# Optimization experiments

Hardware: AMD Instinct MI355X
Metric: run time of the kernel (lower is better)

Reference implementation:

```python
import jax, jax.numpy as jnp
import numpy as np

B, S, D = 2, 2048, 1024
H, HD = 16, 64  # H*HD == D (required by proj layer)
SCALE = D ** -0.5  # NOTE: original scales by full input dim (x.shape[-1]), not head dim


def setup_inputs() -> dict:
    key = jax.random.key(0)
    ks = jax.random.split(key, 7)
    std = D ** -0.5
    x = jax.random.normal(ks[0], (B, S, D), dtype=jnp.float32)
    # per-head projection weights, stacked: [H, D, HD] so x @ Wq[h] == Linear(D->HD)
    Wq = jax.random.normal(ks[1], (H, D, HD), dtype=jnp.float32) * std
    Wk = jax.random.normal(ks[2], (H, D, HD), dtype=jnp.float32) * std
    Wv = jax.random.normal(ks[3], (H, D, HD), dtype=jnp.float32) * std
    # output projection Linear(D, D) with bias
    Wp = jax.random.normal(ks[4], (D, D), dtype=jnp.float32) * std
    bp = jax.random.normal(ks[5], (D,), dtype=jnp.float32) * 0.01
    return {"x": x, "Wq": Wq, "Wk": Wk, "Wv": Wv, "Wp": Wp, "bp": bp}


def reference(x, Wq, Wk, Wv, Wp, bp):
    # All heads see the full x (atsp=False path). Dropout in eval mode (identity).
    q = jnp.einsum('bsd,hde->bhse', x, Wq)  # [B,H,S,HD]
    k = jnp.einsum('bsd,hde->bhse', x, Wk)
    v = jnp.einsum('bsd,hde->bhse', x, Wv)
    scores = jnp.einsum('bhse,bhte->bhst', q, k) * SCALE  # [B,H,S,S]
    causal = jnp.tril(jnp.ones((S, S), dtype=bool))
    scores = jnp.where(causal, scores, -jnp.inf)
    attn = jax.nn.softmax(scores, axis=-1)
    out = jnp.einsum('bhst,bhte->bhse', attn, v)          # [B,H,S,HD]
    # concat heads along last dim in head order: [B,S,H*HD]
    out = out.transpose(0, 2, 1, 3).reshape(B, S, H * HD)
    return out @ Wp.T + bp
```

## Files before the change

### kernel.cpp

```cpp
#include <hip/hip_runtime.h>

typedef __bf16 bf16x8 __attribute__((ext_vector_type(8)));
typedef __bf16 bf16x4 __attribute__((ext_vector_type(4)));
typedef float f32x4 __attribute__((ext_vector_type(4)));
typedef unsigned short u16;
typedef unsigned int u32;

static constexpr int kS = 2048, kD = 1024, kHD = 64;
static constexpr float kQScale = 0.03125f * 1.44269504f;

__device__ __forceinline__ u16 f2bf(float f) {
  union { float f; u32 u; } v; v.f = f;
  u32 r = v.u + 0x7FFFu + ((v.u >> 16) & 1u);
  return (u16)(r >> 16);
}
__device__ __forceinline__ float bf2f(u16 u) {
  union { u32 u; float f; } v; v.u = ((u32)u) << 16;
  return v.f;
}
__device__ __forceinline__ u32 pk2(float a, float b) {
  return (u32)f2bf(a) | ((u32)f2bf(b) << 16);
}
__device__ __forceinline__ f32x4 mfma16(bf16x8 a, bf16x8 b, f32x4 c) {
  return __builtin_amdgcn_mfma_f32_16x16x32_bf16(a, b, c, 0, 0, 0);
}
__device__ __forceinline__ void gld16(u16* lds, const u16* g) {
  __builtin_amdgcn_global_load_lds(
      (const __attribute__((address_space(1))) u32*)g,
      (__attribute__((address_space(3))) u32*)lds, 16, 0, 0);
}

union Pack8 { u16 u[8]; uint4 v; };

__global__ void detect_dtype_kernel(const u16* __restrict__ xr, int* __restrict__ flag) {
  __shared__ int cnt;
  if (threadIdx.x == 0) cnt = 0;
  __syncthreads();
  int c = 0;
  for (int i = threadIdx.x; i < 2048; i += 256) {
    int ex = (xr[i] >> 7) & 0xFF;
    if (ex >= 134) c++;
  }
  if (c) atomicAdd(&cnt, c);
  __syncthreads();
  if (threadIdx.x == 0) flag[0] = (cnt > 16) ? 1 : 0;
}

__global__ void cast_all_kernel(const void* Wq, const void* Wk, const void* Wv,
                                const void* Wp, const void* x,
                                u16* __restrict__ Wt, u16* __restrict__ Wpb,
                                u16* __restrict__ xb, const int* __restrict__ flag) {
  bool f32m = flag[0] != 0;
  int bid = blockIdx.x;
  int t = threadIdx.x;
  __shared__ float Ts[64][65];
  if (bid < 768) {
    int u = bid >> 4;
    int d0 = (bid & 15) * 64;
    int w = u >> 4, h = u & 15;
    const void* srcv = (w == 0) ? Wq : (w == 1) ? Wk : Wv;
    const float* sf = (const float*)srcv + (size_t)h * kD * kHD;
    const u16*   sb = (const u16*)srcv + (size_t)h * kD * kHD;
    int row = t >> 4;
    int c4 = (t & 15) * 4;
    for (int rr = 0; rr < 64; rr += 16) {
      int r = rr + row;
      if (f32m) {
        float4 v = *(const float4*)&sf[(size_t)(d0 + r) * kHD + c4];
        Ts[r][c4 + 0] = v.x; Ts[r][c4 + 1] = v.y; Ts[r][c4 + 2] = v.z; Ts[r][c4 + 3] = v.w;
      } else {
        const u16* p = &sb[(size_t)(d0 + r) * kHD + c4];
        Ts[r][c4 + 0] = bf2f(p[0]); Ts[r][c4 + 1] = bf2f(p[1]);
        Ts[r][c4 + 2] = bf2f(p[2]); Ts[r][c4 + 3] = bf2f(p[3]);
      }
    }
    __syncthreads();
    for (int rr = 0; rr < 64; rr += 16) {
      int e = rr + row;
      uint2 pk;
      pk.x = pk2(Ts[c4 + 0][e], Ts[c4 + 1][e]);
      pk.y = pk2(Ts[c4 + 2][e], Ts[c4 + 3][e]);
      *(uint2*)&Wt[(size_t)u * (kHD * kD) + (size_t)e * kD + d0 + c4] = pk;
    }
  } else if (bid < 1792) {
    int i = ((bid - 768) * 256 + t) * 4;
    if (f32m) {
      float4 v = *(const float4*)((const float*)Wp + i);
      uint2 pk; pk.x = pk2(v.x, v.y); pk.y = pk2(v.z, v.w);
      *(uint2*)&Wpb[i] = pk;
    } else {
      *(uint2*)&Wpb[i] = *(const uint2*)((const u16*)Wp + i);
    }
  } else {
    size_t i = ((size_t)(bid - 1792) * 256 + t) * 8;
    if (f32m) {
      const float* xf = (const float*)x;
      float4 a = *(const float4*)&xf[i];
      float4 b = *(const float4*)&xf[i + 4];
      Pack8 pk;
      pk.u[0] = f2bf(a.x); pk.u[1] = f2bf(a.y); pk.u[2] = f2bf(a.z); pk.u[3] = f2bf(a.w);
      pk.u[4] = f2bf(b.x); pk.u[5] = f2bf(b.y); pk.u[6] = f2bf(b.z); pk.u[7] = f2bf(b.w);
      *(uint4*)&xb[i] = pk.v;
    } else {
      *(uint4*)&xb[i] = *(const uint4*)((const u16*)x + i);
    }
  }
}

__global__ __launch_bounds__(256) void qkv_gemm_kernel(const u16* __restrict__ xb,
    const u16* __restrict__ Wt, u16* __restrict__ Q, u16* __restrict__ K,
    u16* __restrict__ Vt) {
  int m0 = blockIdx.x * 128;
  int n0 = blockIdx.y * 128;
  int w = (int)(blockIdx.y >> 3);
  const u16 *Ap, *Bp; int a0, b0;
  if (w == 2) { Ap = xb; a0 = m0; Bp = Wt; b0 = n0; }
  else        { Ap = Wt; a0 = n0; Bp = xb; b0 = m0; }
  int t = threadIdx.x;
  int wv = t >> 6, l = t & 63;
  int fr = l & 15, fq = l >> 4;
  int wI = (wv >> 1) * 64, wJ = (wv & 1) * 64;
  __shared__ __align__(16) u16 As[128][64];
  __shared__ __align__(16) u16 Bs[128][64];
  int srow = l >> 3, scol = (l & 7) * 8;
  f32x4 acc[4][4];
#pragma unroll
  for (int ii = 0; ii < 4; ++ii)
#pragma unroll
    for (int jj = 0; jj < 4; ++jj)
      for (int i = 0; i < 4; ++i) acc[ii][jj][i] = 0.f;

  for (int kb = 0; kb < kD / 64; ++kb) {
    int k0 = kb * 64;
    __syncthreads();
#pragma unroll
    for (int j = 0; j < 4; ++j) {
      int row = (wv * 4 + j) * 8 + srow;
      gld16(&As[row][scol], &Ap[(size_t)(a0 + row) * kD + k0 + scol]);
      gld16(&Bs[row][scol], &Bp[(size_t)(b0 + row) * kD + k0 + scol]);
    }
    __syncthreads();
    bf16x8 af[4][2], bg[4][2];
#pragma unroll
    for (int ii = 0; ii < 4; ++ii) {
      af[ii][0] = *(const bf16x8*)&As[wI + ii * 16 + fr][fq * 8];
      af[ii][1] = *(const bf16x8*)&As[wI + ii * 16 + fr][32 + fq * 8];
    }
#pragma unroll
    for (int jj = 0; jj < 4; ++jj) {
      bg[jj][0] = *(const bf16x8*)&Bs[wJ + jj * 16 + fr][fq * 8];
      bg[jj][1] = *(const bf16x8*)&Bs[wJ + jj * 16 + fr][32 + fq * 8];
    }
#pragma unroll
    for (int ii = 0; ii < 4; ++ii)
#pragma unroll
      for (int jj = 0; jj < 4; ++jj) {
        acc[ii][jj] = mfma16(af[ii][0], bg[jj][0], acc[ii][jj]);
        acc[ii][jj] = mfma16(af[ii][1], bg[jj][1], acc[ii][jj]);
      }
  }

  if (w == 2) {
    int uh = wv & 1;
    int u = 2 * blockIdx.y + uh;
    int h = u & 15;
#pragma unroll
    for (int jj = 0; jj < 4; ++jj) {
      int e = jj * 16 + fr;
#pragma unroll
      for (int ii = 0; ii < 4; ++ii) {
        int m = m0 + wI + ii * 16 + fq * 4;
        int b = m >> 11, s0 = m & 2047;
        int bh = b * 16 + h;
        *(bf16x4*)&Vt[((size_t)bh * kHD + e) * kS + s0] =
            __builtin_convertvector(acc[ii][jj], bf16x4);
      }
    }
  } else {
    int uh = wv >> 1;
    int u = 2 * blockIdx.y + uh;
    int h = u & 15;
    bool isQ = (w == 0);
    u16* dst = isQ ? Q : K;
#pragma unroll
    for (int jj = 0; jj < 4; ++jj) {
      int m = m0 + wJ + jj * 16 + fr;
      int b = m >> 11, s = m & 2047;
      int bh = b * 16 + h;
      size_t rowb = ((size_t)bh * kS + s) * kHD;
#pragma unroll
      for (int ii = 0; ii < 4; ++ii) {
        int e0 = ii * 16 + fq * 4;
        f32x4 v = acc[ii][jj];
        if (isQ) v *= kQScale;
        *(bf16x4*)&dst[rowb + e0] = __builtin_convertvector(v, bf16x4);
      }
    }
  }
}

__global__ __launch_bounds__(256) void attn_kernel(const u16* __restrict__ Q,
    const u16* __restrict__ K, const u16* __restrict__ Vt, u16* __restrict__ cat) {
  int qb = 31 - (int)(blockIdx.x >> 5);
  int bh = (int)(blockIdx.x & 31);
  int q0 = qb * 64;
  int t = threadIdx.x;
  int wv = t >> 6, l = t & 63;
  int fr = l & 15, fq = l >> 4;
  __shared__ __align__(16) u16 Ks[64][72];
  __shared__ __align__(16) u16 Vs[64][72];
  __shared__ __align__(16) u16 Ps[4][16][72];
  const u16* Qb = Q + (size_t)bh * kS * kHD;
  const u16* Kb = K + (size_t)bh * kS * kHD;
  const u16* Vb = Vt + (size_t)bh * kHD * kS;

  int qrow = q0 + wv * 16 + fr;
  bf16x8 qf0 = *(const bf16x8*)&Qb[(size_t)qrow * kHD + fq * 8];
  bf16x8 qf1 = *(const bf16x8*)&Qb[(size_t)qrow * kHD + 32 + fq * 8];

  f32x4 O[4];
#pragma unroll
  for (int nt = 0; nt < 4; ++nt) for (int i = 0; i < 4; ++i) O[nt][i] = 0.f;
  float lsum = 0.f;

  int srow0 = t >> 3, scol = (t & 7) * 8;
  int srow1 = srow0 + 32;
  uint4 kr0 = *(const uint4*)&Kb[(size_t)srow0 * kHD + scol];
  uint4 kr1 = *(const uint4*)&Kb[(size_t)srow1 * kHD + scol];
  uint4 vr0 = *(const uint4*)&Vb[(size_t)srow0 * kS + scol];
  uint4 vr1 = *(const uint4*)&Vb[(size_t)srow1 * kS + scol];

  for (int tt = 0; tt <= qb; ++tt) {
    int t0 = tt * 64;
    __syncthreads();
    *(uint4*)&Ks[srow0][scol] = kr0;
    *(uint4*)&Ks[srow1][scol] = kr1;
    *(uint4*)&Vs[srow0][scol] = vr0;
    *(uint4*)&Vs[srow1][scol] = vr1;
    __syncthreads();
    if (tt < qb) {
      int t0n = t0 + 64;
      kr0 = *(const uint4*)&Kb[(size_t)(t0n + srow0) * kHD + scol];
      kr1 = *(const uint4*)&Kb[(size_t)(t0n + srow1) * kHD + scol];
      vr0 = *(const uint4*)&Vb[(size_t)srow0 * kS + t0n + scol];
      vr1 = *(const uint4*)&Vb[(size_t)srow1 * kS + t0n + scol];
    }
    f32x4 sc[4];
#pragma unroll
    for (int nt = 0; nt < 4; ++nt) {
      f32x4 z; z[0] = z[1] = z[2] = z[3] = 0.f;
      bf16x8 a0 = *(const bf16x8*)&Ks[nt * 16 + fr][fq * 8];
      bf16x8 a1 = *(const bf16x8*)&Ks[nt * 16 + fr][32 + fq * 8];
      z = mfma16(a0, qf0, z);
      z = mfma16(a1, qf1, z);
      sc[nt] = z;
    }
    if (tt == qb) {
#pragma unroll
      for (int nt = 0; nt < 4; ++nt)
#pragma unroll
        for (int r = 0; r < 4; ++r)
          if (t0 + nt * 16 + fq * 4 + r > qrow) sc[nt][r] = -__builtin_inff();
    }
#pragma unroll
    for (int nt = 0; nt < 4; ++nt) {
#pragma unroll
      for (int r = 0; r < 4; ++r) {
        float p = exp2f(sc[nt][r]);
        sc[nt][r] = p;
        lsum += p;
      }
      *(bf16x4*)&Ps[wv][fr][nt * 16 + fq * 4] = __builtin_convertvector(sc[nt], bf16x4);
    }
    bf16x8 pf0 = *(const bf16x8*)&Ps[wv][fr][fq * 8];
    bf16x8 pf1 = *(const bf16x8*)&Ps[wv][fr][32 + fq * 8];
#pragma unroll
    for (int nt = 0; nt < 4; ++nt) {
      bf16x8 v0 = *(const bf16x8*)&Vs[nt * 16 + fr][fq * 8];
      bf16x8 v1 = *(const bf16x8*)&Vs[nt * 16 + fr][32 + fq * 8];
      O[nt] = mfma16(v0, pf0, O[nt]);
      O[nt] = mfma16(v1, pf1, O[nt]);
    }
  }
  lsum += __shfl_xor(lsum, 16, 64);
  lsum += __shfl_xor(lsum, 32, 64);
  float inv = 1.0f / lsum;
  int b = bh >> 4, h = bh & 15;
  size_t rowbase = ((size_t)(b * kS + qrow)) * kD + h * kHD;
#pragma unroll
  for (int nt = 0; nt < 4; ++nt) {
    f32x4 ov = O[nt] * inv;
    *(bf16x4*)&cat[rowbase + nt * 16 + fq * 4] = __builtin_convertvector(ov, bf16x4);
  }
}

__global__ __launch_bounds__(256) void out_gemm_kernel(const u16* __restrict__ cat,
    const u16* __restrict__ Wpb, const void* __restrict__ bp, void* __restrict__ out,
    const int* __restrict__ flag) {
  bool f32m = flag[0] != 0;
  int m0 = blockIdx.x * 128;
  int n0 = blockIdx.y * 128;
  int t = threadIdx.x;
  int wv = t >> 6, l = t & 63;
  int fr = l & 15, fq = l >> 4;
  int wI = (wv >> 1) * 64, wJ = (wv & 1) * 64;
  __shared__ __align__(16) u16 As[128][64];
  __shared__ __align__(16) u16 Bs[128][64];
  int srow = l >> 3, scol = (l & 7) * 8;
  f32x4 acc[4][4];
#pragma unroll
  for (int ii = 0; ii < 4; ++ii)
#pragma unroll
    for (int jj = 0; jj < 4; ++jj)
      for (int i = 0; i < 4; ++i) acc[ii][jj][i] = 0.f;

  for (int kb = 0; kb < kD / 64; ++kb) {
    int k0 = kb * 64;
    __syncthreads();
#pragma unroll
    for (int j = 0; j < 4; ++j) {
      int row = (wv * 4 + j) * 8 + srow;
      gld16(&As[row][scol], &Wpb[(size_t)(n0 + row) * kD + k0 + scol]);
      gld16(&Bs[row][scol], &cat[(size_t)(m0 + row) * kD + k0 + scol]);
    }
    __syncthreads();
    bf16x8 af[4][2], bg[4][2];
#pragma unroll
    for (int ii = 0; ii < 4; ++ii) {
      af[ii][0] = *(const bf16x8*)&As[wI + ii * 16 + fr][fq * 8];
      af[ii][1] = *(const bf16x8*)&As[wI + ii * 16 + fr][32 + fq * 8];
    }
#pragma unroll
    for (int jj = 0; jj < 4; ++jj) {
      bg[jj][0] = *(const bf16x8*)&Bs[wJ + jj * 16 + fr][fq * 8];
      bg[jj][1] = *(const bf16x8*)&Bs[wJ + jj * 16 + fr][32 + fq * 8];
    }
#pragma unroll
    for (int ii = 0; ii < 4; ++ii)
#pragma unroll
      for (int jj = 0; jj < 4; ++jj) {
        acc[ii][jj] = mfma16(af[ii][0], bg[jj][0], acc[ii][jj]);
        acc[ii][jj] = mfma16(af[ii][1], bg[jj][1], acc[ii][jj]);
      }
  }
  const float* bpf = (const float*)bp;
  const u16*   bpb = (const u16*)bp;
#pragma unroll
  for (int ii = 0; ii < 4; ++ii) {
    int n = n0 + wI + ii * 16 + fq * 4;
    f32x4 bias;
    if (f32m) bias = *(const f32x4*)&bpf[n];
    else { bias[0] = bf2f(bpb[n]); bias[1] = bf2f(bpb[n + 1]);
           bias[2] = bf2f(bpb[n + 2]); bias[3] = bf2f(bpb[n + 3]); }
#pragma unroll
    for (int jj = 0; jj < 4; ++jj) {
      int m = m0 + wJ + jj * 16 + fr;
      f32x4 v = acc[ii][jj] + bias;
      if (f32m) *(f32x4*)&((float*)out)[(size_t)m * kD + n] = v;
      else      *(bf16x4*)&((u16*)out)[(size_t)m * kD + n] = __builtin_convertvector(v, bf16x4);
    }
  }
}

extern "C" void kernel_launch(void* const* d_in, const int* in_sizes, int n_in,
                              void* d_out, int out_size, void* d_ws, size_t ws_size,
                              hipStream_t stream) {
  const void* x  = d_in[0];
  const void* Wq = d_in[1];
  const void* Wk = d_in[2];
  const void* Wv = d_in[3];
  const void* Wp = d_in[4];
  const void* bp = d_in[5];

  char* ws = (char*)d_ws;
  int* flag = (int*)ws;
  u16* Wt  = (u16*)(ws + 256);
  u16* Wpb = (u16*)(ws + 256 + 6291456);
  u16* Qp  = (u16*)(ws + 256 + 6291456 + 2097152);
  u16* Kp  = Qp  + (size_t)32 * 2048 * 64;
  u16* Vtp = Kp  + (size_t)32 * 2048 * 64;
  u16* xb  = Vtp + (size_t)32 * 2048 * 64;
  u16* cat = xb;

  detect_dtype_kernel<<<1, 256, 0, stream>>>((const u16*)x, flag);
  cast_all_kernel<<<3840, 256, 0, stream>>>(Wq, Wk, Wv, Wp, x, Wt, Wpb, xb, flag);
  qkv_gemm_kernel<<<dim3(32, 24), 256, 0, stream>>>(xb, Wt, Qp, Kp, Vtp);
  attn_kernel<<<1024, 256, 0, stream>>>(Qp, Kp, Vtp, cat);
  out_gemm_kernel<<<dim3(32, 8), 256, 0, stream>>>(cat, Wpb, bp, d_out, flag);
}
```

Baseline: 203.7 us.

## Swizzle GEMM LDS tiles and double query rows per attention block with direct K/V loads

Both GEMM kernels now store LDS tiles with an XOR swizzle: each thread fetches a swizzled global column and writes it to a linear LDS slot, and fragment reads apply the same XOR. This is meant to remove bank conflicts on the MFMA fragment reads. The attention kernel now handles 128 query rows per block as two 64-row sub-tiles that share each K/V tile. It drops the LDS staging and barriers for K and V and loads MFMA fragments straight from global memory into registers. That halves the block count and cuts K/V reloads, at the cost of more registers, no prefetch overlap, and possibly less efficient global access.

```diff
diff --git a/kernel.cpp b/kernel.cpp
--- a/kernel.cpp
+++ b/kernel.cpp
@@ -122,7 +122,10 @@
   int wI = (wv >> 1) * 64, wJ = (wv & 1) * 64;
   __shared__ __align__(16) u16 As[128][64];
   __shared__ __align__(16) u16 Bs[128][64];
-  int srow = l >> 3, scol = (l & 7) * 8;
+  int srow = l >> 3;
+  int scol = (((l & 7) ^ srow)) * 8;
+  int dcol = (l & 7) * 8;
+  int sw = fr & 7;
   f32x4 acc[4][4];
 #pragma unroll
   for (int ii = 0; ii < 4; ++ii)
@@ -136,20 +139,20 @@
 #pragma unroll
     for (int j = 0; j < 4; ++j) {
       int row = (wv * 4 + j) * 8 + srow;
-      gld16(&As[row][scol], &Ap[(size_t)(a0 + row) * kD + k0 + scol]);
-      gld16(&Bs[row][scol], &Bp[(size_t)(b0 + row) * kD + k0 + scol]);
+      gld16(&As[row][dcol], &Ap[(size_t)(a0 + row) * kD + k0 + scol]);
+      gld16(&Bs[row][dcol], &Bp[(size_t)(b0 + row) * kD + k0 + scol]);
     }
     __syncthreads();
     bf16x8 af[4][2], bg[4][2];
 #pragma unroll
     for (int ii = 0; ii < 4; ++ii) {
-      af[ii][0] = *(const bf16x8*)&As[wI + ii * 16 + fr][fq * 8];
-      af[ii][1] = *(const bf16x8*)&As[wI + ii * 16 + fr][32 + fq * 8];
+      af[ii][0] = *(const bf16x8*)&As[wI + ii * 16 + fr][((0 + fq) ^ sw) * 8];
+      af[ii][1] = *(const bf16x8*)&As[wI + ii * 16 + fr][((4 + fq) ^ sw) * 8];
     }
 #pragma unroll
     for (int jj = 0; jj < 4; ++jj) {
-      bg[jj][0] = *(const bf16x8*)&Bs[wJ + jj * 16 + fr][fq * 8];
-      bg[jj][1] = *(const bf16x8*)&Bs[wJ + jj * 16 + fr][32 + fq * 8];
+      bg[jj][0] = *(const bf16x8*)&Bs[wJ + jj * 16 + fr][((0 + fq) ^ sw) * 8];
+      bg[jj][1] = *(const bf16x8*)&Bs[wJ + jj * 16 + fr][((4 + fq) ^ sw) * 8];
     }
 #pragma unroll
     for (int ii = 0; ii < 4; ++ii)
@@ -201,96 +204,130 @@
 
 __global__ __launch_bounds__(256) void attn_kernel(const u16* __restrict__ Q,
     const u16* __restrict__ K, const u16* __restrict__ Vt, u16* __restrict__ cat) {
-  int qb = 31 - (int)(blockIdx.x >> 5);
+  int qb = 15 - (int)(blockIdx.x >> 5);
   int bh = (int)(blockIdx.x & 31);
-  int q0 = qb * 64;
+  int q0 = qb * 128;
   int t = threadIdx.x;
   int wv = t >> 6, l = t & 63;
   int fr = l & 15, fq = l >> 4;
-  __shared__ __align__(16) u16 Ks[64][72];
-  __shared__ __align__(16) u16 Vs[64][72];
-  __shared__ __align__(16) u16 Ps[4][16][72];
+  __shared__ __align__(16) u16 Ps[4][2][16][72];
   const u16* Qb = Q + (size_t)bh * kS * kHD;
   const u16* Kb = K + (size_t)bh * kS * kHD;
   const u16* Vb = Vt + (size_t)bh * kHD * kS;
 
-  int qrow = q0 + wv * 16 + fr;
-  bf16x8 qf0 = *(const bf16x8*)&Qb[(size_t)qrow * kHD + fq * 8];
-  bf16x8 qf1 = *(const bf16x8*)&Qb[(size_t)qrow * kHD + 32 + fq * 8];
-
-  f32x4 O[4];
-#pragma unroll
-  for (int nt = 0; nt < 4; ++nt) for (int i = 0; i < 4; ++i) O[nt][i] = 0.f;
-  float lsum = 0.f;
-
-  int srow0 = t >> 3, scol = (t & 7) * 8;
-  int srow1 = srow0 + 32;
-  uint4 kr0 = *(const uint4*)&Kb[(size_t)srow0 * kHD + scol];
-  uint4 kr1 = *(const uint4*)&Kb[(size_t)srow1 * kHD + scol];
-  uint4 vr0 = *(const uint4*)&Vb[(size_t)srow0 * kS + scol];
-  uint4 vr1 = *(const uint4*)&Vb[(size_t)srow1 * kS + scol];
-
-  for (int tt = 0; tt <= qb; ++tt) {
+  int qrA = q0 + wv * 16 + fr;
+  int qrB = qrA + 64;
+  bf16x8 qA0 = *(const bf16x8*)&Qb[(size_t)qrA * kHD + fq * 8];
+  bf16x8 qA1 = *(const bf16x8*)&Qb[(size_t)qrA * kHD + 32 + fq * 8];
+  bf16x8 qB0 = *(const bf16x8*)&Qb[(size_t)qrB * kHD + fq * 8];
+  bf16x8 qB1 = *(const bf16x8*)&Qb[(size_t)qrB * kHD + 32 + fq * 8];
+
+  f32x4 O[2][4];
+#pragma unroll
+  for (int s = 0; s < 2; ++s)
+#pragma unroll
+    for (int nt = 0; nt < 4; ++nt)
+      for (int i = 0; i < 4; ++i) O[s][nt][i] = 0.f;
+  float lsum[2] = {0.f, 0.f};
+
+  const u16* kl = Kb + (size_t)fr * kHD + fq * 8;
+  const u16* vl = Vb + (size_t)fr * kS + fq * 8;
+
+  int tmax = 2 * qb + 1;
+  for (int tt = 0; tt <= tmax; ++tt) {
     int t0 = tt * 64;
-    __syncthreads();
-    *(uint4*)&Ks[srow0][scol] = kr0;
-    *(uint4*)&Ks[srow1][scol] = kr1;
-    *(uint4*)&Vs[srow0][scol] = vr0;
-    *(uint4*)&Vs[srow1][scol] = vr1;
-    __syncthreads();
-    if (tt < qb) {
-      int t0n = t0 + 64;
-      kr0 = *(const uint4*)&Kb[(size_t)(t0n + srow0) * kHD + scol];
-      kr1 = *(const uint4*)&Kb[(size_t)(t0n + srow1) * kHD + scol];
-      vr0 = *(const uint4*)&Vb[(size_t)srow0 * kS + t0n + scol];
-      vr1 = *(const uint4*)&Vb[(size_t)srow1 * kS + t0n + scol];
-    }
-    f32x4 sc[4];
+    bool doA = (tt < tmax);
+    bf16x8 kf[4][2], vf[4][2];
 #pragma unroll
     for (int nt = 0; nt < 4; ++nt) {
-      f32x4 z; z[0] = z[1] = z[2] = z[3] = 0.f;
-      bf16x8 a0 = *(const bf16x8*)&Ks[nt * 16 + fr][fq * 8];
-      bf16x8 a1 = *(const bf16x8*)&Ks[nt * 16 + fr][32 + fq * 8];
-      z = mfma16(a0, qf0, z);
-      z = mfma16(a1, qf1, z);
-      sc[nt] = z;
-    }
-    if (tt == qb) {
+      const u16* kp = kl + (size_t)(t0 + nt * 16) * kHD;
+      kf[nt][0] = *(const bf16x8*)kp;
+      kf[nt][1] = *(const bf16x8*)(kp + 32);
+      const u16* vp = vl + (size_t)(nt * 16) * kS + t0;
+      vf[nt][0] = *(const bf16x8*)vp;
+      vf[nt][1] = *(const bf16x8*)(vp + 32);
+    }
+    f32x4 scA[4], scB[4];
+#pragma unroll
+    for (int nt = 0; nt < 4; ++nt) {
+      f32x4 zB; zB[0] = zB[1] = zB[2] = zB[3] = 0.f;
+      zB = mfma16(kf[nt][0], qB0, zB);
+      zB = mfma16(kf[nt][1], qB1, zB);
+      scB[nt] = zB;
+      if (doA) {
+        f32x4 zA; zA[0] = zA[1] = zA[2] = zA[3] = 0.f;
+        zA = mfma16(kf[nt][0], qA0, zA);
+        zA = mfma16(kf[nt][1], qA1, zA);
+        scA[nt] = zA;
+      }
+    }
+    if (doA) {
+      if (tt == tmax - 1) {
+#pragma unroll
+        for (int nt = 0; nt < 4; ++nt)
+#pragma unroll
+          for (int r = 0; r < 4; ++r)
+            if (t0 + nt * 16 + fq * 4 + r > qrA) scA[nt][r] = -__builtin_inff();
+      }
+#pragma unroll
+      for (int nt = 0; nt < 4; ++nt) {
+#pragma unroll
+        for (int r = 0; r < 4; ++r) {
+          float p = exp2f(scA[nt][r]);
+          scA[nt][r] = p;
+          lsum[0] += p;
+        }
+        *(bf16x4*)&Ps[wv][0][fr][nt * 16 + fq * 4] = __builtin_convertvector(scA[nt], bf16x4);
+      }
+    }
+    if (tt == tmax) {
 #pragma unroll
       for (int nt = 0; nt < 4; ++nt)
 #pragma unroll
         for (int r = 0; r < 4; ++r)
-          if (t0 + nt * 16 + fq * 4 + r > qrow) sc[nt][r] = -__builtin_inff();
+          if (t0 + nt * 16 + fq * 4 + r > qrB) scB[nt][r] = -__builtin_inff();
     }
 #pragma unroll
     for (int nt = 0; nt < 4; ++nt) {
 #pragma unroll
       for (int r = 0; r < 4; ++r) {
-        float p = exp2f(sc[nt][r]);
-        sc[nt][r] = p;
-        lsum += p;
-      }
-      *(bf16x4*)&Ps[wv][fr][nt * 16 + fq * 4] = __builtin_convertvector(sc[nt], bf16x4);
-    }
-    bf16x8 pf0 = *(const bf16x8*)&Ps[wv][fr][fq * 8];
-    bf16x8 pf1 = *(const bf16x8*)&Ps[wv][fr][32 + fq * 8];
+        float p = exp2f(scB[nt][r]);
+        scB[nt][r] = p;
+        lsum[1] += p;
+      }
+      *(bf16x4*)&Ps[wv][1][fr][nt * 16 + fq * 4] = __builtin_convertvector(scB[nt], bf16x4);
+    }
+    bf16x8 pB0 = *(const bf16x8*)&Ps[wv][1][fr][fq * 8];
+    bf16x8 pB1 = *(const bf16x8*)&Ps[wv][1][fr][32 + fq * 8];
+    bf16x8 pA0, pA1;
+    if (doA) {
+      pA0 = *(const bf16x8*)&Ps[wv][0][fr][fq * 8];
+      pA1 = *(const bf16x8*)&Ps[wv][0][fr][32 + fq * 8];
+    }
 #pragma unroll
     for (int nt = 0; nt < 4; ++nt) {
-      bf16x8 v0 = *(const bf16x8*)&Vs[nt * 16 + fr][fq * 8];
-      bf16x8 v1 = *(const bf16x8*)&Vs[nt * 16 + fr][32 + fq * 8];
-      O[nt] = mfma16(v0, pf0, O[nt]);
-      O[nt] = mfma16(v1, pf1, O[nt]);
-    }
-  }
-  lsum += __shfl_xor(lsum, 16, 64);
-  lsum += __shfl_xor(lsum, 32, 64);
-  float inv = 1.0f / lsum;
+      if (doA) {
+        O[0][nt] = mfma16(vf[nt][0], pA0, O[0][nt]);
+        O[0][nt] = mfma16(vf[nt][1], pA1, O[0][nt]);
+      }
+      O[1][nt] = mfma16(vf[nt][0], pB0, O[1][nt]);
+      O[1][nt] = mfma16(vf[nt][1], pB1, O[1][nt]);
+    }
+  }
   int b = bh >> 4, h = bh & 15;
-  size_t rowbase = ((size_t)(b * kS + qrow)) * kD + h * kHD;
-#pragma unroll
-  for (int nt = 0; nt < 4; ++nt) {
-    f32x4 ov = O[nt] * inv;
-    *(bf16x4*)&cat[rowbase + nt * 16 + fq * 4] = __builtin_convertvector(ov, bf16x4);
+#pragma unroll
+  for (int s = 0; s < 2; ++s) {
+    float ls = lsum[s];
+    ls += __shfl_xor(ls, 16, 64);
+    ls += __shfl_xor(ls, 32, 64);
+    float inv = 1.0f / ls;
+    int qrow = (s == 0) ? qrA : qrB;
+    size_t rowbase = ((size_t)(b * kS + qrow)) * kD + h * kHD;
+#pragma unroll
+    for (int nt = 0; nt < 4; ++nt) {
+      f32x4 ov = O[s][nt] * inv;
+      *(bf16x4*)&cat[rowbase + nt * 16 + fq * 4] = __builtin_convertvector(ov, bf16x4);
+    }
   }
 }
 
@@ -306,7 +343,10 @@
   int wI = (wv >> 1) * 64, wJ = (wv & 1) * 64;
   __shared__ __align__(16) u16 As[128][64];
   __shared__ __align__(16) u16 Bs[128][64];
-  int srow = l >> 3, scol = (l & 7) * 8;
+  int srow = l >> 3;
+  int scol = (((l & 7) ^ srow)) * 8;
+  int dcol = (l & 7) * 8;
+  int sw = fr & 7;
   f32x4 acc[4][4];
 #pragma unroll
   for (int ii = 0; ii < 4; ++ii)
@@ -320,20 +360,20 @@
 #pragma unroll
     for (int j = 0; j < 4; ++j) {
       int row = (wv * 4 + j) * 8 + srow;
-      gld16(&As[row][scol], &Wpb[(size_t)(n0 + row) * kD + k0 + scol]);
-      gld16(&Bs[row][scol], &cat[(size_t)(m0 + row) * kD + k0 + scol]);
+      gld16(&As[row][dcol], &Wpb[(size_t)(n0 + row) * kD + k0 + scol]);
+      gld16(&Bs[row][dcol], &cat[(size_t)(m0 + row) * kD + k0 + scol]);
     }
     __syncthreads();
     bf16x8 af[4][2], bg[4][2];
 #pragma unroll
     for (int ii = 0; ii < 4; ++ii) {
-      af[ii][0] = *(const bf16x8*)&As[wI + ii * 16 + fr][fq * 8];
-      af[ii][1] = *(const bf16x8*)&As[wI + ii * 16 + fr][32 + fq * 8];
+      af[ii][0] = *(const bf16x8*)&As[wI + ii * 16 + fr][((0 + fq) ^ sw) * 8];
+      af[ii][1] = *(const bf16x8*)&As[wI + ii * 16 + fr][((4 + fq) ^ sw) * 8];
     }
 #pragma unroll
     for (int jj = 0; jj < 4; ++jj) {
-      bg[jj][0] = *(const bf16x8*)&Bs[wJ + jj * 16 + fr][fq * 8];
-      bg[jj][1] = *(const bf16x8*)&Bs[wJ + jj * 16 + fr][32 + fq * 8];
+      bg[jj][0] = *(const bf16x8*)&Bs[wJ + jj * 16 + fr][((0 + fq) ^ sw) * 8];
+      bg[jj][1] = *(const bf16x8*)&Bs[wJ + jj * 16 + fr][((4 + fq) ^ sw) * 8];
     }
 #pragma unroll
     for (int ii = 0; ii < 4; ++ii)
@@ -385,6 +425,6 @@
   detect_dtype_kernel<<<1, 256, 0, stream>>>((const u16*)x, flag);
   cast_all_kernel<<<3840, 256, 0, stream>>>(Wq, Wk, Wv, Wp, x, Wt, Wpb, xb, flag);
   qkv_gemm_kernel<<<dim3(32, 24), 256, 0, stream>>>(xb, Wt, Qp, Kp, Vtp);
-  attn_kernel<<<1024, 256, 0, stream>>>(Qp, Kp, Vtp, cat);
+  attn_kernel<<<512, 256, 0, stream>>>(Qp, Kp, Vtp, cat);
   out_gemm_kernel<<<dim3(32, 8), 256, 0, stream>>>(cat, Wpb, bp, d_out, flag);
 }
```

Result: slower. 236.8 us (+16.3%).

## XOR-swizzle LDS tiles in GEMMs and attention; shrink out-GEMM M tile

Applied to the files above, without the earlier changes.

Applies an XOR swizzle to the LDS column index for the QKV GEMM, the out GEMM and the attention K/V tiles, which removes bank conflicts on the MFMA fragment reads. In attention this also drops the padding, so the K/V tiles shrink to 64x64. Separately, the out GEMM M tile is halved to 64 rows, doubling the grid to 512 blocks and improving occupancy across the CUs. The cost is less operand reuse per block in the out GEMM and slightly more index arithmetic.

```diff
diff --git a/kernel.cpp b/kernel.cpp
--- a/kernel.cpp
+++ b/kernel.cpp
@@ -122,7 +122,10 @@
   int wI = (wv >> 1) * 64, wJ = (wv & 1) * 64;
   __shared__ __align__(16) u16 As[128][64];
   __shared__ __align__(16) u16 Bs[128][64];
-  int srow = l >> 3, scol = (l & 7) * 8;
+  int srow = l >> 3;
+  int scol = (((l & 7) ^ srow)) * 8;
+  int dcol = (l & 7) * 8;
+  int sw = fr & 7;
   f32x4 acc[4][4];
 #pragma unroll
   for (int ii = 0; ii < 4; ++ii)
@@ -136,20 +139,20 @@
 #pragma unroll
     for (int j = 0; j < 4; ++j) {
       int row = (wv * 4 + j) * 8 + srow;
-      gld16(&As[row][scol], &Ap[(size_t)(a0 + row) * kD + k0 + scol]);
-      gld16(&Bs[row][scol], &Bp[(size_t)(b0 + row) * kD + k0 + scol]);
+      gld16(&As[row][dcol], &Ap[(size_t)(a0 + row) * kD + k0 + scol]);
+      gld16(&Bs[row][dcol], &Bp[(size_t)(b0 + row) * kD + k0 + scol]);
     }
     __syncthreads();
     bf16x8 af[4][2], bg[4][2];
 #pragma unroll
     for (int ii = 0; ii < 4; ++ii) {
-      af[ii][0] = *(const bf16x8*)&As[wI + ii * 16 + fr][fq * 8];
-      af[ii][1] = *(const bf16x8*)&As[wI + ii * 16 + fr][32 + fq * 8];
+      af[ii][0] = *(const bf16x8*)&As[wI + ii * 16 + fr][((0 + fq) ^ sw) * 8];
+      af[ii][1] = *(const bf16x8*)&As[wI + ii * 16 + fr][((4 + fq) ^ sw) * 8];
     }
 #pragma unroll
     for (int jj = 0; jj < 4; ++jj) {
-      bg[jj][0] = *(const bf16x8*)&Bs[wJ + jj * 16 + fr][fq * 8];
-      bg[jj][1] = *(const bf16x8*)&Bs[wJ + jj * 16 + fr][32 + fq * 8];
+      bg[jj][0] = *(const bf16x8*)&Bs[wJ + jj * 16 + fr][((0 + fq) ^ sw) * 8];
+      bg[jj][1] = *(const bf16x8*)&Bs[wJ + jj * 16 + fr][((4 + fq) ^ sw) * 8];
     }
 #pragma unroll
     for (int ii = 0; ii < 4; ++ii)
@@ -207,8 +210,8 @@
   int t = threadIdx.x;
   int wv = t >> 6, l = t & 63;
   int fr = l & 15, fq = l >> 4;
-  __shared__ __align__(16) u16 Ks[64][72];
-  __shared__ __align__(16) u16 Vs[64][72];
+  __shared__ __align__(16) u16 Ks[64][64];
+  __shared__ __align__(16) u16 Vs[64][64];
   __shared__ __align__(16) u16 Ps[4][16][72];
   const u16* Qb = Q + (size_t)bh * kS * kHD;
   const u16* Kb = K + (size_t)bh * kS * kHD;
@@ -223,12 +226,14 @@
   for (int nt = 0; nt < 4; ++nt) for (int i = 0; i < 4; ++i) O[nt][i] = 0.f;
   float lsum = 0.f;
 
-  int srow0 = t >> 3, scol = (t & 7) * 8;
+  int srow0 = t >> 3, gcol = (t & 7) * 8;
   int srow1 = srow0 + 32;
-  uint4 kr0 = *(const uint4*)&Kb[(size_t)srow0 * kHD + scol];
-  uint4 kr1 = *(const uint4*)&Kb[(size_t)srow1 * kHD + scol];
-  uint4 vr0 = *(const uint4*)&Vb[(size_t)srow0 * kS + scol];
-  uint4 vr1 = *(const uint4*)&Vb[(size_t)srow1 * kS + scol];
+  int scol = (((t & 7) ^ (srow0 & 7))) * 8;
+  int sw = fr & 7;
+  uint4 kr0 = *(const uint4*)&Kb[(size_t)srow0 * kHD + gcol];
+  uint4 kr1 = *(const uint4*)&Kb[(size_t)srow1 * kHD + gcol];
+  uint4 vr0 = *(const uint4*)&Vb[(size_t)srow0 * kS + gcol];
+  uint4 vr1 = *(const uint4*)&Vb[(size_t)srow1 * kS + gcol];
 
   for (int tt = 0; tt <= qb; ++tt) {
     int t0 = tt * 64;
@@ -240,17 +245,17 @@
     __syncthreads();
     if (tt < qb) {
       int t0n = t0 + 64;
-      kr0 = *(const uint4*)&Kb[(size_t)(t0n + srow0) * kHD + scol];
-      kr1 = *(const uint4*)&Kb[(size_t)(t0n + srow1) * kHD + scol];
-      vr0 = *(const uint4*)&Vb[(size_t)srow0 * kS + t0n + scol];
-      vr1 = *(const uint4*)&Vb[(size_t)srow1 * kS + t0n + scol];
+      kr0 = *(const uint4*)&Kb[(size_t)(t0n + srow0) * kHD + gcol];
+      kr1 = *(const uint4*)&Kb[(size_t)(t0n + srow1) * kHD + gcol];
+      vr0 = *(const uint4*)&Vb[(size_t)srow0 * kS + t0n + gcol];
+      vr1 = *(const uint4*)&Vb[(size_t)srow1 * kS + t0n + gcol];
     }
     f32x4 sc[4];
 #pragma unroll
     for (int nt = 0; nt < 4; ++nt) {
       f32x4 z; z[0] = z[1] = z[2] = z[3] = 0.f;
-      bf16x8 a0 = *(const bf16x8*)&Ks[nt * 16 + fr][fq * 8];
-      bf16x8 a1 = *(const bf16x8*)&Ks[nt * 16 + fr][32 + fq * 8];
+      bf16x8 a0 = *(const bf16x8*)&Ks[nt * 16 + fr][((0 + fq) ^ sw) * 8];
+      bf16x8 a1 = *(const bf16x8*)&Ks[nt * 16 + fr][((4 + fq) ^ sw) * 8];
       z = mfma16(a0, qf0, z);
       z = mfma16(a1, qf1, z);
       sc[nt] = z;
@@ -276,8 +281,8 @@
     bf16x8 pf1 = *(const bf16x8*)&Ps[wv][fr][32 + fq * 8];
 #pragma unroll
     for (int nt = 0; nt < 4; ++nt) {
-      bf16x8 v0 = *(const bf16x8*)&Vs[nt * 16 + fr][fq * 8];
-      bf16x8 v1 = *(const bf16x8*)&Vs[nt * 16 + fr][32 + fq * 8];
+      bf16x8 v0 = *(const bf16x8*)&Vs[nt * 16 + fr][((0 + fq) ^ sw) * 8];
+      bf16x8 v1 = *(const bf16x8*)&Vs[nt * 16 + fr][((4 + fq) ^ sw) * 8];
       O[nt] = mfma16(v0, pf0, O[nt]);
       O[nt] = mfma16(v1, pf1, O[nt]);
     }
@@ -298,20 +303,23 @@
     const u16* __restrict__ Wpb, const void* __restrict__ bp, void* __restrict__ out,
     const int* __restrict__ flag) {
   bool f32m = flag[0] != 0;
-  int m0 = blockIdx.x * 128;
+  int m0 = blockIdx.x * 64;
   int n0 = blockIdx.y * 128;
   int t = threadIdx.x;
   int wv = t >> 6, l = t & 63;
   int fr = l & 15, fq = l >> 4;
-  int wI = (wv >> 1) * 64, wJ = (wv & 1) * 64;
+  int wI = (wv >> 1) * 64, wJ = (wv & 1) * 32;
   __shared__ __align__(16) u16 As[128][64];
-  __shared__ __align__(16) u16 Bs[128][64];
-  int srow = l >> 3, scol = (l & 7) * 8;
-  f32x4 acc[4][4];
+  __shared__ __align__(16) u16 Bs[64][64];
+  int srow = l >> 3;
+  int scol = (((l & 7) ^ srow)) * 8;
+  int dcol = (l & 7) * 8;
+  int sw = fr & 7;
+  f32x4 acc[4][2];
 #pragma unroll
   for (int ii = 0; ii < 4; ++ii)
 #pragma unroll
-    for (int jj = 0; jj < 4; ++jj)
+    for (int jj = 0; jj < 2; ++jj)
       for (int i = 0; i < 4; ++i) acc[ii][jj][i] = 0.f;
 
   for (int kb = 0; kb < kD / 64; ++kb) {
@@ -319,26 +327,30 @@
     __syncthreads();
 #pragma unroll
     for (int j = 0; j < 4; ++j) {
-      int row = (wv * 4 + j) * 8 + srow;
-      gld16(&As[row][scol], &Wpb[(size_t)(n0 + row) * kD + k0 + scol]);
-      gld16(&Bs[row][scol], &cat[(size_t)(m0 + row) * kD + k0 + scol]);
-    }
-    __syncthreads();
-    bf16x8 af[4][2], bg[4][2];
+      int row = j * 32 + wv * 8 + srow;
+      gld16(&As[row][dcol], &Wpb[(size_t)(n0 + row) * kD + k0 + scol]);
+    }
+#pragma unroll
+    for (int j = 0; j < 2; ++j) {
+      int row = j * 32 + wv * 8 + srow;
+      gld16(&Bs[row][dcol], &cat[(size_t)(m0 + row) * kD + k0 + scol]);
+    }
+    __syncthreads();
+    bf16x8 af[4][2], bg[2][2];
 #pragma unroll
     for (int ii = 0; ii < 4; ++ii) {
-      af[ii][0] = *(const bf16x8*)&As[wI + ii * 16 + fr][fq * 8];
-      af[ii][1] = *(const bf16x8*)&As[wI + ii * 16 + fr][32 + fq * 8];
-    }
-#pragma unroll
-    for (int jj = 0; jj < 4; ++jj) {
-      bg[jj][0] = *(const bf16x8*)&Bs[wJ + jj * 16 + fr][fq * 8];
-      bg[jj][1] = *(const bf16x8*)&Bs[wJ + jj * 16 + fr][32 + fq * 8];
+      af[ii][0] = *(const bf16x8*)&As[wI + ii * 16 + fr][((0 + fq) ^ sw) * 8];
+      af[ii][1] = *(const bf16x8*)&As[wI + ii * 16 + fr][((4 + fq) ^ sw) * 8];
+    }
+#pragma unroll
+    for (int jj = 0; jj < 2; ++jj) {
+      bg[jj][0] = *(const bf16x8*)&Bs[wJ + jj * 16 + fr][((0 + fq) ^ sw) * 8];
+      bg[jj][1] = *(const bf16x8*)&Bs[wJ + jj * 16 + fr][((4 + fq) ^ sw) * 8];
     }
 #pragma unroll
     for (int ii = 0; ii < 4; ++ii)
 #pragma unroll
-      for (int jj = 0; jj < 4; ++jj) {
+      for (int jj = 0; jj < 2; ++jj) {
         acc[ii][jj] = mfma16(af[ii][0], bg[jj][0], acc[ii][jj]);
         acc[ii][jj] = mfma16(af[ii][1], bg[jj][1], acc[ii][jj]);
       }
@@ -353,7 +365,7 @@
     else { bias[0] = bf2f(bpb[n]); bias[1] = bf2f(bpb[n + 1]);
            bias[2] = bf2f(bpb[n + 2]); bias[3] = bf2f(bpb[n + 3]); }
 #pragma unroll
-    for (int jj = 0; jj < 4; ++jj) {
+    for (int jj = 0; jj < 2; ++jj) {
       int m = m0 + wJ + jj * 16 + fr;
       f32x4 v = acc[ii][jj] + bias;
       if (f32m) *(f32x4*)&((float*)out)[(size_t)m * kD + n] = v;
@@ -386,5 +398,5 @@
   cast_all_kernel<<<3840, 256, 0, stream>>>(Wq, Wk, Wv, Wp, x, Wt, Wpb, xb, flag);
   qkv_gemm_kernel<<<dim3(32, 24), 256, 0, stream>>>(xb, Wt, Qp, Kp, Vtp);
   attn_kernel<<<1024, 256, 0, stream>>>(Qp, Kp, Vtp, cat);
-  out_gemm_kernel<<<dim3(32, 8), 256, 0, stream>>>(cat, Wpb, bp, d_out, flag);
-}
+  out_gemm_kernel<<<dim3(64, 8), 256, 0, stream>>>(cat, Wpb, bp, d_out, flag);
+}
```

Result: faster. 175.8 us (-13.7%).
